# Kernel optimization log

Hardware: AMD Instinct MI355X
Metric: run time of the kernel (lower is better)

Reference implementation:

```python
import math
import jax, jax.numpy as jnp
import numpy as np

C, H, W = 128, 64, 64
R, K = 7, 3          # 7x3 dilated window
PAD_H, PAD_W = 9, 2  # from unfold paddings
DIL_H, DIL_W = 3, 2  # row/col dilations


def _neighborhood(x):
    """Gather dilated 7x3 neighborhood: out[n,c,r,k,i,j] = x[n,c, i+3r-9, j+2k-2] (zero-padded).
    x: (n,c,h,w) -> (n,c,7,3,h,w)."""
    n, c, h, w = x.shape
    xp = jnp.pad(x, ((0, 0), (0, 0), (PAD_H, PAD_H), (PAD_W, PAD_W)))
    taps = [xp[:, :, DIL_H * r:DIL_H * r + h, DIL_W * k:DIL_W * k + w]
            for r in range(R) for k in range(K)]
    return jnp.stack(taps, axis=2).reshape(n, c, R, K, h, w)


def setup_inputs() -> dict:
    key = jax.random.key(0)
    k1, k2, k3 = jax.random.split(key, 3)
    x = jax.random.normal(k1, (4, C, H, W), dtype=jnp.float32)
    p5_w = 0.1 * jax.random.normal(k2, (1, C, R, K, H, W), dtype=jnp.float32)
    p6_w = 0.1 * jax.random.normal(k3, (1, C, R, K, C), dtype=jnp.float32)
    return {"x": x, "p5_w": p5_w, "p6_w": p6_w}


def reference(x, p5_w, p6_w):
    n, c, h, w = x.shape
    # t_2: dilated 7x3 neighborhood gather (double unfold)
    t2 = _neighborhood(x)                                   # (n,c,7,3,h,w)
    # t_3: bmm((n,c*21,hw), (n,hw,c)) / sqrt(hw)
    t3 = jnp.einsum('ncrkhw,ndhw->ncrkd', t2, x) / math.sqrt(h * w)  # (n,c,7,3,c)
    # elementwise modulation
    t7 = p5_w * t2 + t2                                     # (n,c,7,3,h,w)
    t6 = p6_w * t3                                          # (n,c,7,3,c)
    # t_8: bmm((n,hw,c*21), (n,c*21,c)) / sqrt(c*21)
    t8 = jnp.einsum('ncrkhw,ncrkd->nhwd', t7, t6) / math.sqrt(c * R * K)  # (n,h,w,c)
    return jnp.transpose(t8, (0, 3, 1, 2))                  # (n,c,h,w)
```

## Files before the change

### kernel.cpp

```cpp
#include <hip/hip_runtime.h>

typedef _Float16 f16;
typedef _Float16 f16x2 __attribute__((ext_vector_type(2)));
typedef _Float16 f16x4 __attribute__((ext_vector_type(4)));
typedef _Float16 f16x8 __attribute__((ext_vector_type(8)));
typedef float    f32x4 __attribute__((ext_vector_type(4)));

#define XROWS 82
#define XSTR  (XROWS * 64)
#define XK_ELEMS (3u * 4u * 128u * (unsigned)XSTR)
static const size_t T6T_OFF   = (size_t)XK_ELEMS * 2;
static const size_t T6T_BYTES = (size_t)4 * 128 * 2688 * 2;
static const size_t T3P_OFF   = T6T_OFF + T6T_BYTES;
static const size_t T8P_OFF   = T3P_OFF;

__device__ __forceinline__ void gl16(const f16* g, f16* l) {
  __builtin_amdgcn_global_load_lds((const __attribute__((address_space(1))) void*)g,
                                   (__attribute__((address_space(3))) void*)l, 16, 0, 0);
}

__global__ __launch_bounds__(256) void prep_kernel(const float* __restrict__ x,
                                                   f16* __restrict__ xk) {
  unsigned p = blockIdx.x * 256u + threadIdx.x;
  unsigned total = 3u * 4u * 128u * 82u * 32u;
  if (p >= total) return;
  unsigned wp   = p & 31u;
  unsigned row  = (p >> 5) % 82u;
  unsigned rest = p / (32u * 82u);
  unsigned c    = rest & 127u;
  unsigned rest2 = rest >> 7;
  unsigned n    = rest2 & 3u;
  unsigned kc   = rest2 >> 2;
  int hsrc = (int)row - 9;
  int wsrc = (int)(wp * 2u) + 2 * (int)kc - 2;
  f16x2 v; v.x = (f16)0.f; v.y = (f16)0.f;
  if (hsrc >= 0 && hsrc < 64 && wsrc >= 0 && wsrc < 64) {
    const float2* src = (const float2*)(x + (((size_t)(n * 128u + c) * 64u + (unsigned)hsrc) * 64u + (unsigned)wsrc));
    float2 xv = *src;
    v.x = (f16)(xv.x * 0.125f);
    v.y = (f16)(xv.y * 0.125f);
  }
  ((f16x2*)xk)[p] = v;
}

__global__ __launch_bounds__(256, 3) void gram_kernel(const f16* __restrict__ xk,
                                                      f16* __restrict__ t3p) {
  __shared__ f16 gl[2 * 12288];

  unsigned b    = blockIdx.x;
  unsigned ks   = b & 7u;
  unsigned cseg = (b >> 3) & 1u;
  unsigned rki  = (b >> 4) % 11u;
  unsigned n    = b / 176u;
  unsigned r    = rki / 3u;
  unsigned kc   = rki - r * 3u;

  unsigned tid  = threadIdx.x;
  unsigned wv   = tid >> 6;
  unsigned lane = tid & 63u;
  unsigned wy   = wv >> 1;
  unsigned wx   = wv & 1u;
  unsigned quad = lane >> 4;
  unsigned l16  = lane & 15u;
  unsigned rsl  = lane >> 3;
  unsigned seg  = (lane & 7u) ^ (rsl & 7u);

  unsigned h0 = ks * 8u;
  const f16* Ab = xk + (size_t)(kc * 4u + n) * 128u * XSTR + (size_t)(cseg * 64u) * XSTR
                + (h0 + 3u * r) * 64u + seg * 8u;
  const f16* Bb = xk + (size_t)(4u + n) * 128u * XSTR + (h0 + 9u) * 64u + seg * 8u;
  unsigned ar0 = wv * 16u;
  unsigned br0 = wv * 32u;

  f32x4 acc[2][4] = {};

#pragma unroll
  for (unsigned t = 0; t < 2u; t++)
    gl16(Ab + (size_t)(ar0 + t * 8u + rsl) * XSTR, &gl[(ar0 + t * 8u) * 64u]);
#pragma unroll
  for (unsigned t = 0; t < 4u; t++)
    gl16(Bb + (size_t)(br0 + t * 8u + rsl) * XSTR, &gl[4096u + (br0 + t * 8u) * 64u]);

  for (unsigned s = 0; s < 8u; s++) {
    __syncthreads();
    if (s < 7u) {
      f16* base = &gl[((s + 1u) & 1u) * 12288u];
      unsigned off = (s + 1u) * 64u;
#pragma unroll
      for (unsigned t = 0; t < 2u; t++)
        gl16(Ab + off + (size_t)(ar0 + t * 8u + rsl) * XSTR, base + (ar0 + t * 8u) * 64u);
#pragma unroll
      for (unsigned t = 0; t < 4u; t++)
        gl16(Bb + off + (size_t)(br0 + t * 8u + rsl) * XSTR, base + 4096u + (br0 + t * 8u) * 64u);
    }
    const f16* bufA = &gl[(s & 1u) * 12288u];
    const f16* bufB = bufA + 4096u;
#pragma unroll
    for (unsigned t2 = 0; t2 < 2u; t2++) {
      unsigned L = t2 * 4u + quad;
      f16x8 a[2], bb[4];
#pragma unroll
      for (int ms = 0; ms < 2; ms++) {
        unsigned rr = wy * 32u + (unsigned)ms * 16u + l16;
        a[ms] = *(const f16x8*)&bufA[rr * 64u + (L ^ (rr & 7u)) * 8u];
      }
#pragma unroll
      for (int ns = 0; ns < 4; ns++) {
        unsigned rb = wx * 64u + (unsigned)ns * 16u + l16;
        bb[ns] = *(const f16x8*)&bufB[rb * 64u + (L ^ (rb & 7u)) * 8u];
      }
#pragma unroll
      for (int ms = 0; ms < 2; ms++)
#pragma unroll
        for (int ns = 0; ns < 4; ns++)
          acc[ms][ns] = __builtin_amdgcn_mfma_f32_16x16x32_f16(a[ms], bb[ns], acc[ms][ns], 0, 0, 0);
    }
  }

  f16* tp = t3p + ((size_t)(ks * 4u + n) * 11u + rki) * 16384u;
#pragma unroll
  for (int ms = 0; ms < 2; ms++) {
#pragma unroll
    for (int ns = 0; ns < 4; ns++) {
      unsigned c0 = cseg * 64u + wy * 32u + (unsigned)ms * 16u + quad * 4u;
      unsigned d  = wx * 64u + (unsigned)ns * 16u + l16;
#pragma unroll
      for (int reg = 0; reg < 4; reg++)
        tp[(size_t)(c0 + (unsigned)reg) * 128u + d] = (f16)acc[ms][ns][reg];
    }
  }
}

__global__ __launch_bounds__(256) void ep_kernel(const f16* __restrict__ t3p,
                                                 const float* __restrict__ p6,
                                                 f16* __restrict__ t6B) {
  unsigned idx = blockIdx.x * 256u + threadIdx.x;
  unsigned t   = idx >> 12;
  unsigned rk  = t % 21u;
  unsigned n   = t / 21u;
  f16* tb = t6B + (size_t)t * 16384u;

  if (rk <= 10u) {
    unsigned d4 = idx & 31u;
    unsigned c  = (idx >> 5) & 127u;
    unsigned d0 = d4 * 4u;
    float s0 = 0.f, s1 = 0.f, s2 = 0.f, s3 = 0.f;
#pragma unroll
    for (unsigned ks = 0; ks < 8u; ks++) {
      f16x4 v = *(const f16x4*)(t3p + (((size_t)(ks * 4u + n) * 11u + rk) * 16384u + c * 128u + d0));
      s0 += (float)v[0]; s1 += (float)v[1]; s2 += (float)v[2]; s3 += (float)v[3];
    }
    const float* pp = p6 + ((size_t)c * 21u + rk) * 128u + d0;
    f16* ob = tb + (c >> 5) * 4096u + (d0 >> 4) * 512u + ((c >> 3) & 3u) * 128u + (d0 & 15u) * 8u + (c & 7u);
    ob[0]  = (f16)(s0 * pp[0]);
    ob[8]  = (f16)(s1 * pp[1]);
    ob[16] = (f16)(s2 * pp[2]);
    ob[24] = (f16)(s3 * pp[3]);
  } else {
    unsigned mrk = 20u - rk;
    unsigned c4 = idx & 31u;
    unsigned d  = (idx >> 5) & 127u;
    unsigned c0 = c4 * 4u;
    float s0 = 0.f, s1 = 0.f, s2 = 0.f, s3 = 0.f;
#pragma unroll
    for (unsigned ks = 0; ks < 8u; ks++) {
      f16x4 v = *(const f16x4*)(t3p + (((size_t)(ks * 4u + n) * 11u + mrk) * 16384u + d * 128u + c0));
      s0 += (float)v[0]; s1 += (float)v[1]; s2 += (float)v[2]; s3 += (float)v[3];
    }
    f16x4 o;
    o[0] = (f16)(s0 * p6[((size_t)(c0 + 0u) * 21u + rk) * 128u + d]);
    o[1] = (f16)(s1 * p6[((size_t)(c0 + 1u) * 21u + rk) * 128u + d]);
    o[2] = (f16)(s2 * p6[((size_t)(c0 + 2u) * 21u + rk) * 128u + d]);
    o[3] = (f16)(s3 * p6[((size_t)(c0 + 3u) * 21u + rk) * 128u + d]);
    *(f16x4*)(tb + (c0 >> 5) * 4096u + (d >> 4) * 512u + ((c0 >> 3) & 3u) * 128u + (d & 15u) * 8u + (c0 & 7u)) = o;
  }
}

#define ALDS_STR 40
#define RT_STR   66
__global__ __launch_bounds__(512, 8) void outp_kernel(const f16* __restrict__ xk,
                                                      const float* __restrict__ p5,
                                                      const f16* __restrict__ t6B,
                                                      f16* __restrict__ t8p) {
  __shared__ float smem[8448];
  f16* Alds = (f16*)smem;

  unsigned b = blockIdx.x;
  unsigned g = b & 3u;
  unsigned h = (b >> 2) & 63u;
  unsigned n = b >> 8;

  unsigned tid  = threadIdx.x;
  unsigned wv   = tid >> 6;
  unsigned lane = tid & 63u;
  unsigned wy   = wv >> 2;
  unsigned wx   = wv & 3u;
  unsigned quad = lane >> 4;
  unsigned l16  = lane & 15u;
  unsigned wst  = tid & 63u;
  unsigned g8   = tid >> 6;
  unsigned cth  = g * 32u + g8 * 4u;

  const float* prow0 = p5 + (size_t)cth * (21u * 4096u) + h * 64u + wst;
  const f16* t6b = t6B + (size_t)n * 344064u + g * 4096u + (size_t)lane * 8u;

  f32x4 acc[2][2] = {};
  f16 xv[4]; float pv[4];
  f16x8 bfc[2];

  {
    const f16* xrow = xk + (((size_t)n * 128u + cth) * XROWS + h) * 64u + wst;
#pragma unroll
    for (int i = 0; i < 4; i++) { xv[i] = xrow[(size_t)i * XSTR]; pv[i] = prow0[(size_t)i * (21u * 4096u)]; }
#pragma unroll
    for (int ns = 0; ns < 2; ns++) bfc[ns] = *(const f16x8*)(t6b + (wx * 2u + (unsigned)ns) * 512u);
  }

  for (unsigned j = 0; j < 21u; j++) {
    f16* Ag = Alds + (j & 1u) * 2560u;
    {
      f16x4 av;
#pragma unroll
      for (int i = 0; i < 4; i++) av[i] = (f16)((float)xv[i] * (1.0f + pv[i]));
      *(f16x4*)&Ag[wst * ALDS_STR + g8 * 4u] = av;
    }
    __syncthreads();

    f16x8 bfn[2];
    if (j < 20u) {
      unsigned rk = j + 1u;
      unsigned rr = rk / 3u;
      unsigned kcc = rk - rr * 3u;
      const f16* xrow = xk + (((size_t)(kcc * 4u + n) * 128u + cth) * XROWS + (h + 3u * rr)) * 64u + wst;
      const float* prow = prow0 + rk * 4096u;
#pragma unroll
      for (int i = 0; i < 4; i++) { xv[i] = xrow[(size_t)i * XSTR]; pv[i] = prow[(size_t)i * (21u * 4096u)]; }
#pragma unroll
      for (int ns = 0; ns < 2; ns++) bfn[ns] = *(const f16x8*)(t6b + rk * 16384u + (wx * 2u + (unsigned)ns) * 512u);
    }

    f16x8 a[2];
#pragma unroll
    for (int ms = 0; ms < 2; ms++)
      a[ms] = *(const f16x8*)&Ag[(wy * 32u + (unsigned)ms * 16u + l16) * ALDS_STR + quad * 8u];
#pragma unroll
    for (int ms = 0; ms < 2; ms++)
#pragma unroll
      for (int ns = 0; ns < 2; ns++)
        acc[ms][ns] = __builtin_amdgcn_mfma_f32_16x16x32_f16(a[ms], bfc[ns], acc[ms][ns], 0, 0, 0);
#pragma unroll
    for (int ns = 0; ns < 2; ns++) bfc[ns] = bfn[ns];
  }

  __syncthreads();
  float* Rt = smem;
#pragma unroll
  for (int ms = 0; ms < 2; ms++)
#pragma unroll
    for (int ns = 0; ns < 2; ns++) {
      unsigned w0 = wy * 32u + (unsigned)ms * 16u + quad * 4u;
      unsigned d  = wx * 32u + (unsigned)ns * 16u + l16;
#pragma unroll
      for (int reg = 0; reg < 4; reg++)
        Rt[d * RT_STR + w0 + (unsigned)reg] = acc[ms][ns][reg];
    }
  __syncthreads();
  f16* op = t8p + ((size_t)((g * 4u + n) * 64u + h)) * 8192u;
  {
    unsigned row = tid >> 2;
    unsigned w0  = (tid & 3u) * 16u;
    f16x8 o0, o1;
#pragma unroll
    for (int i = 0; i < 8; i++) {
      o0[i] = (f16)Rt[row * RT_STR + w0 + (unsigned)i];
      o1[i] = (f16)Rt[row * RT_STR + w0 + 8u + (unsigned)i];
    }
    *(f16x8*)(op + row * 64u + w0) = o0;
    *(f16x8*)(op + row * 64u + w0 + 8u) = o1;
  }
}

__global__ __launch_bounds__(256) void red_kernel(const f16* __restrict__ t8p,
                                                  float* __restrict__ out) {
  unsigned idx = blockIdx.x * 256u + threadIdx.x;
  unsigned w0 = (idx & 7u) * 8u;
  unsigned h  = (idx >> 3) & 63u;
  unsigned d  = (idx >> 9) & 127u;
  unsigned n  = idx >> 16;
  const float FS = 0.15430334996209192f;
  float s[8] = {};
#pragma unroll
  for (unsigned g = 0; g < 4u; g++) {
    f16x8 v = *(const f16x8*)(t8p + ((size_t)((g * 4u + n) * 64u + h)) * 8192u + d * 64u + w0);
#pragma unroll
    for (int i = 0; i < 8; i++) s[i] += (float)v[i];
  }
  f32x4 o0, o1;
#pragma unroll
  for (int i = 0; i < 4; i++) { o0[i] = s[i] * FS; o1[i] = s[i + 4] * FS; }
  float* op = out + ((size_t)(n * 128u + d) * 64u + h) * 64u + w0;
  *(f32x4*)op = o0;
  *(f32x4*)(op + 4) = o1;
}

extern "C" void kernel_launch(void* const* d_in, const int* in_sizes, int n_in,
                              void* d_out, int out_size, void* d_ws, size_t ws_size,
                              hipStream_t stream) {
  const float* x  = (const float*)d_in[0];
  const float* p5 = (const float*)d_in[1];
  const float* p6 = (const float*)d_in[2];
  float* out = (float*)d_out;
  f16* xk  = (f16*)((char*)d_ws);
  f16* t6B = (f16*)((char*)d_ws + T6T_OFF);
  f16* t3p = (f16*)((char*)d_ws + T3P_OFF);
  f16* t8p = (f16*)((char*)d_ws + T8P_OFF);

  unsigned prep_blocks = (3u * 4u * 128u * 82u * 32u + 255u) / 256u;
  hipLaunchKernelGGL(prep_kernel, dim3(prep_blocks), dim3(256), 0, stream, x, xk);
  hipLaunchKernelGGL(gram_kernel, dim3(704),  dim3(256), 0, stream, xk, t3p);
  hipLaunchKernelGGL(ep_kernel,   dim3(1344), dim3(256), 0, stream, t3p, p6, t6B);
  hipLaunchKernelGGL(outp_kernel, dim3(1024), dim3(512), 0, stream, xk, p5, t6B, t8p);
  hipLaunchKernelGGL(red_kernel,  dim3(1024), dim3(256), 0, stream, t8p, out);
}
```

Measured before the change: 149.3 us.

## Stage t6 B-operand through LDS via async global_load_lds, halve A-staging threads

The outp kernel now loads the t6 B fragments into a double-buffered LDS region with direct global-to-LDS loads instead of per-wave register prefetch, which removes duplicate global reads across waves sharing the same B tile. A staging is reduced to the first 256 threads, each handling 8 channels and writing one f16x8, into an XOR-swizzled LDS layout that replaces the padded-stride layout. This trades fewer redundant B loads and wider A stores against less thread parallelism for the p5/x modulation and extra LDS reads for B. It relies on the existing barrier to order the async LDS fills.

```diff
diff --git a/kernel.cpp b/kernel.cpp
--- a/kernel.cpp
+++ b/kernel.cpp
@@ -176,14 +176,13 @@
   }
 }
 
-#define ALDS_STR 40
 #define RT_STR   66
 __global__ __launch_bounds__(512, 8) void outp_kernel(const f16* __restrict__ xk,
                                                       const float* __restrict__ p5,
                                                       const f16* __restrict__ t6B,
                                                       f16* __restrict__ t8p) {
   __shared__ float smem[8448];
-  f16* Alds = (f16*)smem;
+  f16* sm16 = (f16*)smem;
 
   unsigned b = blockIdx.x;
   unsigned g = b & 3u;
@@ -198,58 +197,66 @@
   unsigned quad = lane >> 4;
   unsigned l16  = lane & 15u;
   unsigned wst  = tid & 63u;
-  unsigned g8   = tid >> 6;
-  unsigned cth  = g * 32u + g8 * 4u;
+  bool     stg  = (tid < 256u);
+  unsigned cg8  = tid >> 6;
+  unsigned cth  = g * 32u + cg8 * 8u;
 
   const float* prow0 = p5 + (size_t)cth * (21u * 4096u) + h * 64u + wst;
-  const f16* t6b = t6B + (size_t)n * 344064u + g * 4096u + (size_t)lane * 8u;
+  const f16* t6base = t6B + (size_t)n * 344064u + g * 4096u;
 
   f32x4 acc[2][2] = {};
-  f16 xv[4]; float pv[4];
-  f16x8 bfc[2];
+  f16 xv[8]; float pv[8];
 
   {
-    const f16* xrow = xk + (((size_t)n * 128u + cth) * XROWS + h) * 64u + wst;
-#pragma unroll
-    for (int i = 0; i < 4; i++) { xv[i] = xrow[(size_t)i * XSTR]; pv[i] = prow0[(size_t)i * (21u * 4096u)]; }
-#pragma unroll
-    for (int ns = 0; ns < 2; ns++) bfc[ns] = *(const f16x8*)(t6b + (wx * 2u + (unsigned)ns) * 512u);
+    if (stg) {
+      const f16* xrow = xk + (((size_t)n * 128u + cth) * XROWS + h) * 64u + wst;
+#pragma unroll
+      for (int i = 0; i < 8; i++) { xv[i] = xrow[(size_t)i * XSTR]; pv[i] = prow0[(size_t)i * (21u * 4096u)]; }
+    }
+    gl16(t6base + (size_t)tid * 8u, sm16 + 4096u + tid * 8u);
   }
 
   for (unsigned j = 0; j < 21u; j++) {
-    f16* Ag = Alds + (j & 1u) * 2560u;
-    {
-      f16x4 av;
-#pragma unroll
-      for (int i = 0; i < 4; i++) av[i] = (f16)((float)xv[i] * (1.0f + pv[i]));
-      *(f16x4*)&Ag[wst * ALDS_STR + g8 * 4u] = av;
+    f16* Ag = sm16 + (j & 1u) * 2048u;
+    const f16* Bg = sm16 + 4096u + (j & 1u) * 4096u;
+    if (stg) {
+      f16x8 av;
+#pragma unroll
+      for (int i = 0; i < 8; i++) av[i] = (f16)((float)xv[i] * (1.0f + pv[i]));
+      unsigned gr = ((wst & 1u) << 2) | cg8;
+      *(f16x8*)&Ag[(wst >> 1) * 64u + (gr ^ ((wst >> 1) & 7u)) * 8u] = av;
     }
     __syncthreads();
 
-    f16x8 bfn[2];
     if (j < 20u) {
       unsigned rk = j + 1u;
-      unsigned rr = rk / 3u;
-      unsigned kcc = rk - rr * 3u;
-      const f16* xrow = xk + (((size_t)(kcc * 4u + n) * 128u + cth) * XROWS + (h + 3u * rr)) * 64u + wst;
-      const float* prow = prow0 + rk * 4096u;
-#pragma unroll
-      for (int i = 0; i < 4; i++) { xv[i] = xrow[(size_t)i * XSTR]; pv[i] = prow[(size_t)i * (21u * 4096u)]; }
-#pragma unroll
-      for (int ns = 0; ns < 2; ns++) bfn[ns] = *(const f16x8*)(t6b + rk * 16384u + (wx * 2u + (unsigned)ns) * 512u);
-    }
-
-    f16x8 a[2];
+      gl16(t6base + (size_t)rk * 16384u + tid * 8u,
+           sm16 + 4096u + (rk & 1u) * 4096u + tid * 8u);
+      if (stg) {
+        unsigned rr = rk / 3u;
+        unsigned kcc = rk - rr * 3u;
+        const f16* xrow = xk + (((size_t)(kcc * 4u + n) * 128u + cth) * XROWS + (h + 3u * rr)) * 64u + wst;
+        const float* prow = prow0 + rk * 4096u;
+#pragma unroll
+        for (int i = 0; i < 8; i++) { xv[i] = xrow[(size_t)i * XSTR]; pv[i] = prow[(size_t)i * (21u * 4096u)]; }
+      }
+    }
+
+    f16x8 a[2], bfr[2];
+#pragma unroll
+    for (int ms = 0; ms < 2; ms++) {
+      unsigned rr = wy * 32u + (unsigned)ms * 16u + l16;
+      unsigned gr = ((rr & 1u) << 2) | quad;
+      a[ms] = *(const f16x8*)&Ag[(rr >> 1) * 64u + (gr ^ ((rr >> 1) & 7u)) * 8u];
+    }
+#pragma unroll
+    for (int ns = 0; ns < 2; ns++)
+      bfr[ns] = *(const f16x8*)&Bg[(wx * 2u + (unsigned)ns) * 512u + lane * 8u];
 #pragma unroll
     for (int ms = 0; ms < 2; ms++)
-      a[ms] = *(const f16x8*)&Ag[(wy * 32u + (unsigned)ms * 16u + l16) * ALDS_STR + quad * 8u];
-#pragma unroll
-    for (int ms = 0; ms < 2; ms++)
 #pragma unroll
       for (int ns = 0; ns < 2; ns++)
-        acc[ms][ns] = __builtin_amdgcn_mfma_f32_16x16x32_f16(a[ms], bfc[ns], acc[ms][ns], 0, 0, 0);
-#pragma unroll
-    for (int ns = 0; ns < 2; ns++) bfc[ns] = bfn[ns];
+        acc[ms][ns] = __builtin_amdgcn_mfma_f32_16x16x32_f16(a[ms], bfr[ns], acc[ms][ns], 0, 0, 0);
   }
 
   __syncthreads();
```

After: 144.4 us. -3.3%, faster.
